# Kernel tuning notes

Measured on AMD Instinct MI355X. Metric: run time of the kernel, lower is better.

Reference implementation:

```python
import jax, jax.numpy as jnp
import numpy as np

NUM_ITERATIONS = 3

def squash(s, axis=-1):
    # s * ||s||^2 / (1 + ||s||^2) / ||s||
    sq_norm = jnp.sum(s * s, axis=axis, keepdims=True)
    return s * sq_norm / ((1.0 + sq_norm) * jnp.sqrt(sq_norm + 1e-9))


def setup_inputs() -> dict:
    key = jax.random.key(0)
    k1, k2 = jax.random.split(key)
    B, P, J, D_in, D_out = 256, 1152, 10, 8, 16
    x = jax.random.normal(k1, (B, P, D_in), dtype=jnp.float32)
    W = jax.random.normal(k2, (J, D_out, D_in), dtype=jnp.float32)
    return {"x": x, "W": W}


def reference(x, W):
    # u_hat[b,p,j,d] = W[j,d,k] @ x[b,p,k]  (broadcast of W over batch and prim caps)
    u_hat = jnp.einsum('jdk,bpk->bpjd', W, x)  # [B,P,J,D_out]
    B, P, J, _ = u_hat.shape
    b_ij = jnp.zeros((B, P, J), dtype=u_hat.dtype)
    v = None
    for i in range(NUM_ITERATIONS):
        # softmax over primary-capsule axis (dim=1 in the torch code)
        c_ij = jax.nn.softmax(b_ij, axis=1)           # [B,P,J]
        s_j = jnp.einsum('bpj,bpjd->bjd', c_ij, u_hat)  # [B,J,D_out]
        v = squash(s_j, axis=-1)                      # [B,J,D_out]
        if i != NUM_ITERATIONS - 1:
            # agreement: u_hat^T . v
            b_ij = b_ij + jnp.einsum('bpjd,bjd->bpj', u_hat, v)
    return v  # [B, num_digit_cap, out_cap_dim]
```

## Files before the change

### kernel.cpp

```cpp
#include <hip/hip_runtime.h>

#define B_   256
#define P_   1152
#define J_   10
#define NT   384
#define NWV  6
#define PW   192
#define LOG2E 1.44269504088896340736f

typedef __attribute__((ext_vector_type(8))) short short8;
typedef __attribute__((ext_vector_type(4))) float f32x4;

union Frag { short8 s; unsigned u[4]; };

__device__ __forceinline__ unsigned pk_bf16(float lo, float hi) {
  unsigned r;
  asm("v_cvt_pk_bf16_f32 %0, %1, %2" : "=v"(r) : "v"(lo), "v"(hi));
  return r;
}
__device__ __forceinline__ float bf_lo(unsigned u){ return __builtin_bit_cast(float, u << 16); }
__device__ __forceinline__ float bf_hi(unsigned u){ return __builtin_bit_cast(float, u & 0xffff0000u); }

template<int CTRL>
__device__ __forceinline__ float dpp_add(float v) {
  int s = __builtin_amdgcn_update_dpp(0, __builtin_bit_cast(int, v), CTRL, 0xF, 0xF, true);
  return v + __builtin_bit_cast(float, s);
}
__device__ __forceinline__ float rsum_shr(float v) {
  v = dpp_add<0x111>(v); v = dpp_add<0x112>(v);
  v = dpp_add<0x114>(v); v = dpp_add<0x118>(v);
  return v;
}
__device__ __forceinline__ float rsum_ror(float v) {
  v = dpp_add<0x121>(v); v = dpp_add<0x122>(v);
  v = dpp_add<0x124>(v); v = dpp_add<0x128>(v);
  return v;
}

__global__ __launch_bounds__(NT, 2) void caps_kernel(const float* __restrict__ x,
                                                     const float* __restrict__ Wg,
                                                     float* __restrict__ out) {
  extern __shared__ char smc[];
  short* xT    = (short*)smc;
  short* eL    = (short*)(smc + 37376);
  float* Wt    = (float*)(smc + 75776);
  float* ypart = (float*)(smc + 81536);
  float* red   = (float*)(smc + 88064);
  float* Zacc  = (float*)(smc + 88432);

  const int tid  = threadIdx.x;
  const int w    = tid >> 6;
  const int lane = tid & 63;
  const int b    = blockIdx.x;
  const int jl   = lane & 15;
  const int g    = lane >> 4;

  {
    float4* xTf = (float4*)xT;
    const float4 z4 = make_float4(0.f, 0.f, 0.f, 0.f);
    for (int i = tid; i < 2336; i += NT) xTf[i] = z4;
    if (tid < 128) Zacc[tid] = 0.f;
  }
  __syncthreads();

  const float* xb = x + (size_t)b * (P_ * 8);
  for (int i = tid; i < 2304; i += NT) {
    float4 v4 = ((const float4*)xb)[i];
    const int p = i >> 1, k0 = (i & 1) * 4;
    xT[(k0 + 0) * 1168 + p] = (short)(pk_bf16(v4.x, v4.x) & 0xffff);
    xT[(k0 + 1) * 1168 + p] = (short)(pk_bf16(v4.y, v4.y) & 0xffff);
    xT[(k0 + 2) * 1168 + p] = (short)(pk_bf16(v4.z, v4.z) & 0xffff);
    xT[(k0 + 3) * 1168 + p] = (short)(pk_bf16(v4.w, v4.w) & 0xffff);
  }
  for (int p = tid; p < P_; p += NT) xT[8 * 1168 + p] = (short)0x3F80;
  for (int t = tid; t < 1280; t += NT) {
    const int j = t >> 7, d = (t >> 3) & 15, k = t & 7;
    Wt[(j * 8 + k) * 18 + d] = Wg[t];
  }

  Frag Ax[12];
  {
    const bool lop = (g & 1);
    #pragma unroll
    for (int t = 0; t < 12; ++t) {
      const float* xr = xb + ((size_t)(w * PW + t * 16 + jl)) * 8;
      const float4 a4 = ((const float4*)xr)[0];
      const float4 b4 = ((const float4*)xr)[1];
      const float xv[8] = {a4.x, a4.y, a4.z, a4.w, b4.x, b4.y, b4.z, b4.w};
      #pragma unroll
      for (int q = 0; q < 4; ++q) {
        unsigned h = pk_bf16(xv[2 * q], xv[2 * q + 1]);
        if (lop) {
          const float l0 = xv[2 * q]     - bf_lo(h);
          const float l1 = xv[2 * q + 1] - bf_hi(h);
          h = pk_bf16(l0, l1);
        }
        Ax[t].u[q] = h;
      }
    }
  }
  __syncthreads();

  Frag Bx[6];
  #pragma unroll
  for (int tp = 0; tp < 6; ++tp)
    Bx[tp].s = *(const short8*)&xT[jl * 1168 + w * PW + tp * 32 + g * 8];

  Frag ones;
  #pragma unroll
  for (int q = 0; q < 4; ++q) ones.u[q] = 0x3F803F80u;

  for (int it = 0; it < 3; ++it) {
    f32x4 yC = {0.f, 0.f, 0.f, 0.f};
    if (it == 0) {
      #pragma unroll
      for (int tp = 0; tp < 6; ++tp)
        yC = __builtin_amdgcn_mfma_f32_16x16x32_bf16(ones.s, Bx[tp].s, yC, 0, 0, 0);
    } else {
      Frag zf;
      {
        const float4 za = *(const float4*)&Zacc[jl * 8];
        const float4 zb = *(const float4*)&Zacc[jl * 8 + 4];
        const float zv[8] = {za.x, za.y, za.z, za.w, zb.x, zb.y, zb.z, zb.w};
        #pragma unroll
        for (int q = 0; q < 4; ++q) {
          unsigned h = pk_bf16(zv[2 * q], zv[2 * q + 1]);
          if (g >= 2) {
            const float l0 = zv[2 * q]     - bf_lo(h);
            const float l1 = zv[2 * q + 1] - bf_hi(h);
            h = pk_bf16(l0, l1);
          }
          zf.u[q] = h;
        }
      }
      short* eW = eL + w * 3200;
      #pragma unroll
      for (int t = 0; t < 12; ++t) {
        f32x4 bC = {0.f, 0.f, 0.f, 0.f};
        bC = __builtin_amdgcn_mfma_f32_16x16x32_bf16(Ax[t].s, zf.s, bC, 0, 0, 0);
        const float e0 = exp2f(bC[0]), e1 = exp2f(bC[1]);
        const float e2 = exp2f(bC[2]), e3 = exp2f(bC[3]);
        *(uint2*)&eW[jl * 200 + t * 16 + g * 4] =
            make_uint2(pk_bf16(e0, e1), pk_bf16(e2, e3));
      }
      #pragma unroll
      for (int tp = 0; tp < 6; ++tp) {
        Frag af;
        af.s = *(const short8*)&eW[jl * 200 + tp * 32 + g * 8];
        yC = __builtin_amdgcn_mfma_f32_16x16x32_bf16(af.s, Bx[tp].s, yC, 0, 0, 0);
      }
    }
    #pragma unroll
    for (int r = 0; r < 4; ++r)
      ypart[w * 272 + (g * 4 + r) * 17 + jl] = yC[r];
    __syncthreads();

    if (tid < 160) {
      const int j = tid >> 4, k = tid & 15;
      if (k < 9) {
        float s = 0.f;
        #pragma unroll
        for (int w6 = 0; w6 < NWV; ++w6) s += ypart[w6 * 272 + j * 17 + k];
        red[(k < 8) ? (j * 8 + k) : (80 + j)] = s;
      }
    }
    __syncthreads();

    if (tid < 160) {
      const int j = tid >> 4, d = tid & 15;
      float wk[8];
      #pragma unroll
      for (int k = 0; k < 8; ++k) wk[k] = Wt[(j * 8 + k) * 18 + d];
      float s = 0.f;
      #pragma unroll
      for (int k = 0; k < 8; ++k) s = fmaf(wk[k], red[j * 8 + k], s);
      s /= red[80 + j];
      const float sq = rsum_ror(s * s);
      const float scal = sq / ((1.0f + sq) * sqrtf(sq + 1e-9f));
      const float v = s * scal;
      if (it == 2) {
        out[b * 160 + tid] = v;
      } else {
        float zk[8];
        #pragma unroll
        for (int k = 0; k < 8; ++k) zk[k] = rsum_shr(wk[k] * v);
        if (d == 15) {
          #pragma unroll
          for (int k = 0; k < 8; ++k)
            Zacc[j * 8 + k] = fmaf(zk[k], LOG2E, Zacc[j * 8 + k]);
        }
      }
    }
    if (it < 2) __syncthreads();
  }
}

extern "C" void kernel_launch(void* const* d_in, const int* in_sizes, int n_in,
                              void* d_out, int out_size, void* d_ws, size_t ws_size,
                              hipStream_t stream) {
  (void)in_sizes; (void)n_in; (void)out_size; (void)d_ws; (void)ws_size;
  const float* x = (const float*)d_in[0];
  const float* W = (const float*)d_in[1];
  float* out = (float*)d_out;

  const size_t smem = 88944;
  (void)hipFuncSetAttribute(reinterpret_cast<const void*>(caps_kernel),
                            hipFuncAttributeMaxDynamicSharedMemorySize, (int)smem);
  caps_kernel<<<B_, NT, smem, stream>>>(x, W, out);
}
```

Baseline: 15.53 us.

## Double waves per block and replace partial-sum reduction with LDS atomics

Doubles the block to 12 waves, each handling 96 primary capsules, which halves per-wave register fragments and the per-iteration MFMA chain. Cross-wave reduction of the per-wave partial sums now uses LDS atomicAdd into the reduction buffer instead of a staged partial buffer plus a separate reduce pass and barrier. Shared memory shrinks (no initial zero-fill, smaller exp buffer writing only valid rows), and the launch-bounds hint rises to 3 blocks per CU. The costs are atomic contention on a small set of addresses and extra zeroing of the reduction buffer between iterations.

```diff
diff --git a/kernel.cpp b/kernel.cpp
--- a/kernel.cpp
+++ b/kernel.cpp
@@ -3,9 +3,12 @@
 #define B_   256
 #define P_   1152
 #define J_   10
-#define NT   384
-#define NWV  6
-#define PW   192
+#define NT   768
+#define NWV  12
+#define PW   96
+#define XSTR 1176
+#define ESTR 100
+#define EWV  1000
 #define LOG2E 1.44269504088896340736f
 
 typedef __attribute__((ext_vector_type(8))) short short8;
@@ -37,16 +40,15 @@
   return v;
 }
 
-__global__ __launch_bounds__(NT, 2) void caps_kernel(const float* __restrict__ x,
+__global__ __launch_bounds__(NT, 3) void caps_kernel(const float* __restrict__ x,
                                                      const float* __restrict__ Wg,
                                                      float* __restrict__ out) {
   extern __shared__ char smc[];
-  short* xT    = (short*)smc;
-  short* eL    = (short*)(smc + 37376);
-  float* Wt    = (float*)(smc + 75776);
-  float* ypart = (float*)(smc + 81536);
-  float* red   = (float*)(smc + 88064);
-  float* Zacc  = (float*)(smc + 88432);
+  short* xT   = (short*)smc;
+  short* eL   = (short*)(smc + 21168);
+  float* Wt   = (float*)(smc + 45168);
+  float* red  = (float*)(smc + 50928);
+  float* Zacc = (float*)(smc + 51296);
 
   const int tid  = threadIdx.x;
   const int w    = tid >> 6;
@@ -55,34 +57,27 @@
   const int jl   = lane & 15;
   const int g    = lane >> 4;
 
-  {
-    float4* xTf = (float4*)xT;
-    const float4 z4 = make_float4(0.f, 0.f, 0.f, 0.f);
-    for (int i = tid; i < 2336; i += NT) xTf[i] = z4;
-    if (tid < 128) Zacc[tid] = 0.f;
-  }
-  __syncthreads();
-
   const float* xb = x + (size_t)b * (P_ * 8);
   for (int i = tid; i < 2304; i += NT) {
     float4 v4 = ((const float4*)xb)[i];
     const int p = i >> 1, k0 = (i & 1) * 4;
-    xT[(k0 + 0) * 1168 + p] = (short)(pk_bf16(v4.x, v4.x) & 0xffff);
-    xT[(k0 + 1) * 1168 + p] = (short)(pk_bf16(v4.y, v4.y) & 0xffff);
-    xT[(k0 + 2) * 1168 + p] = (short)(pk_bf16(v4.z, v4.z) & 0xffff);
-    xT[(k0 + 3) * 1168 + p] = (short)(pk_bf16(v4.w, v4.w) & 0xffff);
-  }
-  for (int p = tid; p < P_; p += NT) xT[8 * 1168 + p] = (short)0x3F80;
+    xT[(k0 + 0) * XSTR + p] = (short)(pk_bf16(v4.x, v4.x) & 0xffff);
+    xT[(k0 + 1) * XSTR + p] = (short)(pk_bf16(v4.y, v4.y) & 0xffff);
+    xT[(k0 + 2) * XSTR + p] = (short)(pk_bf16(v4.z, v4.z) & 0xffff);
+    xT[(k0 + 3) * XSTR + p] = (short)(pk_bf16(v4.w, v4.w) & 0xffff);
+  }
+  for (int p = tid; p < P_; p += NT) xT[8 * XSTR + p] = (short)0x3F80;
   for (int t = tid; t < 1280; t += NT) {
     const int j = t >> 7, d = (t >> 3) & 15, k = t & 7;
     Wt[(j * 8 + k) * 18 + d] = Wg[t];
   }
-
-  Frag Ax[12];
+  if (tid < 92) red[tid] = 0.f;
+
+  Frag Ax[6];
   {
     const bool lop = (g & 1);
     #pragma unroll
-    for (int t = 0; t < 12; ++t) {
+    for (int t = 0; t < 6; ++t) {
       const float* xr = xb + ((size_t)(w * PW + t * 16 + jl)) * 8;
       const float4 a4 = ((const float4*)xr)[0];
       const float4 b4 = ((const float4*)xr)[1];
@@ -101,10 +96,10 @@
   }
   __syncthreads();
 
-  Frag Bx[6];
+  Frag Bx[3];
   #pragma unroll
-  for (int tp = 0; tp < 6; ++tp)
-    Bx[tp].s = *(const short8*)&xT[jl * 1168 + w * PW + tp * 32 + g * 8];
+  for (int tp = 0; tp < 3; ++tp)
+    Bx[tp].s = *(const short8*)&xT[jl * XSTR + w * PW + tp * 32 + g * 8];
 
   Frag ones;
   #pragma unroll
@@ -114,7 +109,7 @@
     f32x4 yC = {0.f, 0.f, 0.f, 0.f};
     if (it == 0) {
       #pragma unroll
-      for (int tp = 0; tp < 6; ++tp)
+      for (int tp = 0; tp < 3; ++tp)
         yC = __builtin_amdgcn_mfma_f32_16x16x32_bf16(ones.s, Bx[tp].s, yC, 0, 0, 0);
     } else {
       Frag zf;
@@ -133,35 +128,30 @@
           zf.u[q] = h;
         }
       }
-      short* eW = eL + w * 3200;
-      #pragma unroll
-      for (int t = 0; t < 12; ++t) {
+      short* eW = eL + w * EWV;
+      #pragma unroll
+      for (int t = 0; t < 6; ++t) {
         f32x4 bC = {0.f, 0.f, 0.f, 0.f};
         bC = __builtin_amdgcn_mfma_f32_16x16x32_bf16(Ax[t].s, zf.s, bC, 0, 0, 0);
         const float e0 = exp2f(bC[0]), e1 = exp2f(bC[1]);
         const float e2 = exp2f(bC[2]), e3 = exp2f(bC[3]);
-        *(uint2*)&eW[jl * 200 + t * 16 + g * 4] =
-            make_uint2(pk_bf16(e0, e1), pk_bf16(e2, e3));
-      }
-      #pragma unroll
-      for (int tp = 0; tp < 6; ++tp) {
+        if (jl < J_)
+          *(uint2*)&eW[jl * ESTR + t * 16 + g * 4] =
+              make_uint2(pk_bf16(e0, e1), pk_bf16(e2, e3));
+      }
+      #pragma unroll
+      for (int tp = 0; tp < 3; ++tp) {
         Frag af;
-        af.s = *(const short8*)&eW[jl * 200 + tp * 32 + g * 8];
+        af.s = *(const short8*)&eW[jl * ESTR + tp * 32 + g * 8];
         yC = __builtin_amdgcn_mfma_f32_16x16x32_bf16(af.s, Bx[tp].s, yC, 0, 0, 0);
       }
     }
-    #pragma unroll
-    for (int r = 0; r < 4; ++r)
-      ypart[w * 272 + (g * 4 + r) * 17 + jl] = yC[r];
-    __syncthreads();
-
-    if (tid < 160) {
-      const int j = tid >> 4, k = tid & 15;
-      if (k < 9) {
-        float s = 0.f;
-        #pragma unroll
-        for (int w6 = 0; w6 < NWV; ++w6) s += ypart[w6 * 272 + j * 17 + k];
-        red[(k < 8) ? (j * 8 + k) : (80 + j)] = s;
+    if (jl < 9) {
+      #pragma unroll
+      for (int r = 0; r < 4; ++r) {
+        const int j = g * 4 + r;
+        if (j < J_)
+          atomicAdd(&red[(jl < 8) ? (j * 8 + jl) : (80 + j)], yC[r]);
       }
     }
     __syncthreads();
@@ -187,8 +177,11 @@
         if (d == 15) {
           #pragma unroll
           for (int k = 0; k < 8; ++k)
-            Zacc[j * 8 + k] = fmaf(zk[k], LOG2E, Zacc[j * 8 + k]);
+            Zacc[j * 8 + k] = (it == 0) ? zk[k] * LOG2E
+                                        : fmaf(zk[k], LOG2E, Zacc[j * 8 + k]);
         }
+        if (d < 8)        red[j * 8 + d] = 0.f;
+        else if (d == 8)  red[80 + j]    = 0.f;
       }
     }
     if (it < 2) __syncthreads();
@@ -203,7 +196,7 @@
   const float* W = (const float*)d_in[1];
   float* out = (float*)d_out;
 
-  const size_t smem = 88944;
+  const size_t smem = 51840;
   (void)hipFuncSetAttribute(reinterpret_cast<const void*>(caps_kernel),
                             hipFuncAttributeMaxDynamicSharedMemorySize, (int)smem);
   caps_kernel<<<B_, NT, smem, stream>>>(x, W, out);
```

After: 17.59 us. 13.3% more time.

## Fuse xT staging into fragment load and merge reduction phases to cut barriers

Applied to the files above, without the earlier changes.

Builds the transposed bf16 copy of x in LDS from the registers already loaded for the A fragments, which removes the separate global pass, the zero-fill of xT and its barrier. The cross-wave reduction is merged into the squash phase, so each thread sums ypart directly and one barrier per iteration disappears. Zacc is written on the first iteration instead of being pre-zeroed, and the xT stride changes, shrinking shared memory. Rows 9-15 of xT are no longer zeroed, so the B fragment reads for those rows pick up uninitialised LDS. Those rows only feed unused output columns, but this is a correctness risk if that assumption fails.

```diff
diff --git a/kernel.cpp b/kernel.cpp
--- a/kernel.cpp
+++ b/kernel.cpp
@@ -6,6 +6,7 @@
 #define NT   384
 #define NWV  6
 #define PW   192
+#define XSTR 1176
 #define LOG2E 1.44269504088896340736f
 
 typedef __attribute__((ext_vector_type(8))) short short8;
@@ -42,11 +43,10 @@
                                                      float* __restrict__ out) {
   extern __shared__ char smc[];
   short* xT    = (short*)smc;
-  short* eL    = (short*)(smc + 37376);
-  float* Wt    = (float*)(smc + 75776);
-  float* ypart = (float*)(smc + 81536);
-  float* red   = (float*)(smc + 88064);
-  float* Zacc  = (float*)(smc + 88432);
+  short* eL    = (short*)(smc + 21168);
+  float* Wt    = (float*)(smc + 59568);
+  float* ypart = (float*)(smc + 65328);
+  float* Zacc  = (float*)(smc + 71856);
 
   const int tid  = threadIdx.x;
   const int w    = tid >> 6;
@@ -55,35 +55,21 @@
   const int jl   = lane & 15;
   const int g    = lane >> 4;
 
-  {
-    float4* xTf = (float4*)xT;
-    const float4 z4 = make_float4(0.f, 0.f, 0.f, 0.f);
-    for (int i = tid; i < 2336; i += NT) xTf[i] = z4;
-    if (tid < 128) Zacc[tid] = 0.f;
-  }
-  __syncthreads();
-
   const float* xb = x + (size_t)b * (P_ * 8);
-  for (int i = tid; i < 2304; i += NT) {
-    float4 v4 = ((const float4*)xb)[i];
-    const int p = i >> 1, k0 = (i & 1) * 4;
-    xT[(k0 + 0) * 1168 + p] = (short)(pk_bf16(v4.x, v4.x) & 0xffff);
-    xT[(k0 + 1) * 1168 + p] = (short)(pk_bf16(v4.y, v4.y) & 0xffff);
-    xT[(k0 + 2) * 1168 + p] = (short)(pk_bf16(v4.z, v4.z) & 0xffff);
-    xT[(k0 + 3) * 1168 + p] = (short)(pk_bf16(v4.w, v4.w) & 0xffff);
-  }
-  for (int p = tid; p < P_; p += NT) xT[8 * 1168 + p] = (short)0x3F80;
+
   for (int t = tid; t < 1280; t += NT) {
     const int j = t >> 7, d = (t >> 3) & 15, k = t & 7;
     Wt[(j * 8 + k) * 18 + d] = Wg[t];
   }
+  if (tid < 48) Zacc[80 + tid] = 0.f;
 
   Frag Ax[12];
   {
     const bool lop = (g & 1);
     #pragma unroll
     for (int t = 0; t < 12; ++t) {
-      const float* xr = xb + ((size_t)(w * PW + t * 16 + jl)) * 8;
+      const int p = w * PW + t * 16 + jl;
+      const float* xr = xb + (size_t)p * 8;
       const float4 a4 = ((const float4*)xr)[0];
       const float4 b4 = ((const float4*)xr)[1];
       const float xv[8] = {a4.x, a4.y, a4.z, a4.w, b4.x, b4.y, b4.z, b4.w};
@@ -97,6 +83,17 @@
         }
         Ax[t].u[q] = h;
       }
+      if (g == 0) {
+        #pragma unroll
+        for (int k = 0; k < 4; ++k)
+          xT[k * XSTR + p] = (short)(pk_bf16(xv[k], xv[k]) & 0xffff);
+      } else if (g == 1) {
+        #pragma unroll
+        for (int k = 4; k < 8; ++k)
+          xT[k * XSTR + p] = (short)(pk_bf16(xv[k], xv[k]) & 0xffff);
+      } else if (g == 2) {
+        xT[8 * XSTR + p] = (short)0x3F80;
+      }
     }
   }
   __syncthreads();
@@ -104,7 +101,7 @@
   Frag Bx[6];
   #pragma unroll
   for (int tp = 0; tp < 6; ++tp)
-    Bx[tp].s = *(const short8*)&xT[jl * 1168 + w * PW + tp * 32 + g * 8];
+    Bx[tp].s = *(const short8*)&xT[jl * XSTR + w * PW + tp * 32 + g * 8];
 
   Frag ones;
   #pragma unroll
@@ -156,25 +153,22 @@
     __syncthreads();
 
     if (tid < 160) {
-      const int j = tid >> 4, k = tid & 15;
-      if (k < 9) {
-        float s = 0.f;
-        #pragma unroll
-        for (int w6 = 0; w6 < NWV; ++w6) s += ypart[w6 * 272 + j * 17 + k];
-        red[(k < 8) ? (j * 8 + k) : (80 + j)] = s;
-      }
-    }
-    __syncthreads();
-
-    if (tid < 160) {
       const int j = tid >> 4, d = tid & 15;
+      float yk[9];
+      #pragma unroll
+      for (int k = 0; k < 9; ++k) {
+        float s6 = 0.f;
+        #pragma unroll
+        for (int w6 = 0; w6 < NWV; ++w6) s6 += ypart[w6 * 272 + j * 17 + k];
+        yk[k] = s6;
+      }
       float wk[8];
       #pragma unroll
       for (int k = 0; k < 8; ++k) wk[k] = Wt[(j * 8 + k) * 18 + d];
       float s = 0.f;
       #pragma unroll
-      for (int k = 0; k < 8; ++k) s = fmaf(wk[k], red[j * 8 + k], s);
-      s /= red[80 + j];
+      for (int k = 0; k < 8; ++k) s = fmaf(wk[k], yk[k], s);
+      s /= yk[8];
       const float sq = rsum_ror(s * s);
       const float scal = sq / ((1.0f + sq) * sqrtf(sq + 1e-9f));
       const float v = s * scal;
@@ -187,7 +181,8 @@
         if (d == 15) {
           #pragma unroll
           for (int k = 0; k < 8; ++k)
-            Zacc[j * 8 + k] = fmaf(zk[k], LOG2E, Zacc[j * 8 + k]);
+            Zacc[j * 8 + k] = (it == 0) ? zk[k] * LOG2E
+                                        : fmaf(zk[k], LOG2E, Zacc[j * 8 + k]);
         }
       }
     }
@@ -203,7 +198,7 @@
   const float* W = (const float*)d_in[1];
   float* out = (float*)d_out;
 
-  const size_t smem = 88944;
+  const size_t smem = 72368;
   (void)hipFuncSetAttribute(reinterpret_cast<const void*>(caps_kernel),
                             hipFuncAttributeMaxDynamicSharedMemorySize, (int)smem);
   caps_kernel<<<B_, NT, smem, stream>>>(x, W, out);
```

Result: slower. 16.77 us (+8.0%).
